# Performance work log

Hardware: AMD Instinct MI355X
Metric: run time of the kernel (lower is better)

## Reference

```python
import jax, jax.numpy as jnp
import numpy as np

HIDDEN = 1024
HEADS = 16
HEAD = HIDDEN // HEADS


def setup_inputs() -> dict:
    key = jax.random.key(0)
    k1, k2, k3, k4, k5, k6 = jax.random.split(key, 6)
    B, S = 2, 2048
    x = jax.random.normal(k1, (B, S, HIDDEN), dtype=jnp.float32)
    mask = jax.random.randint(k2, (B, S), 0, 2, dtype=jnp.int32)
    # torch nn.Linear params: W [out,in], b [out]
    s = 1.0 / np.sqrt(HIDDEN)
    qkv_w = jax.random.uniform(k3, (3 * HIDDEN, HIDDEN), jnp.float32, -s, s)
    qkv_b = jax.random.uniform(k4, (3 * HIDDEN,), jnp.float32, -s, s)
    out_w = jax.random.uniform(k5, (HIDDEN, HIDDEN), jnp.float32, -s, s)
    out_b = jax.random.uniform(k6, (HIDDEN,), jnp.float32, -s, s)
    return {"x": x, "mask": mask, "qkv_w": qkv_w, "qkv_b": qkv_b,
            "out_w": out_w, "out_b": out_b}


def reference(x, mask, qkv_w, qkv_b, out_w, out_b):
    B, S, H = x.shape
    scale = HEAD ** -0.5
    qkv = x @ qkv_w.T + qkv_b                      # [B,S,3H]
    qkv = qkv.reshape(B, S, 3, HEADS, HEAD)
    qkv = jnp.transpose(qkv, (2, 0, 3, 1, 4))      # [3,B,h,S,d]
    q, k, v = qkv[0], qkv[1], qkv[2]
    scores = jnp.einsum('bhqd,bhkd->bhqk', q, k) * scale
    # key-padding mask [B,S] -> [B,1,1,S]
    scores = jnp.where(mask[:, None, None, :] == 0, -1e9, scores)
    attn = jax.nn.softmax(scores, axis=-1)
    # dropout is identity in eval mode
    ctx = jnp.einsum('bhqk,bhkd->bhqd', attn, v)   # [B,h,S,d]
    ctx = jnp.transpose(ctx, (0, 2, 1, 3)).reshape(B, S, H)
    return ctx @ out_w.T + out_b
```

## Files before the change

### kernel.cpp

```cpp
#include <hip/hip_runtime.h>
#include <hip/hip_bf16.h>

#define S_LEN 2048
#define NH    16
#define HD    64
#define HID   1024
#define BATCH 2
#define STK   72
#define VSTK  136
#define SCQ   0.18033688f

typedef __bf16 bf16x8 __attribute__((ext_vector_type(8)));
typedef float  f32x4  __attribute__((ext_vector_type(4)));
typedef float  f32x16 __attribute__((ext_vector_type(16)));
typedef unsigned u32x2 __attribute__((ext_vector_type(2)));

__device__ __forceinline__ unsigned int pk2(float lo, float hi) {
    union { __hip_bfloat162 h; unsigned int u; } c;
    c.h = __float22bfloat162_rn(make_float2(lo, hi));
    return c.u;
}
__device__ __forceinline__ uint4 pk8(float4 a, float4 b) {
    uint4 o;
    o.x = pk2(a.x, a.y); o.y = pk2(a.z, a.w);
    o.z = pk2(b.x, b.y); o.w = pk2(b.z, b.w);
    return o;
}
__device__ __forceinline__ float exp2_hw(float x) {
    float r; asm("v_exp_f32 %0, %1" : "=v"(r) : "v"(x)); return r;
}
__device__ __forceinline__ void pl32swap(unsigned &a, unsigned &b) {
    u32x2 r = __builtin_amdgcn_permlane32_swap(a, b, false, false);
    a = r[0]; b = r[1];
}
__device__ __forceinline__ float pair_max(float x) {
    unsigned u = __float_as_uint(x);
    u32x2 r = __builtin_amdgcn_permlane32_swap(u, u, false, false);
    return fmaxf(__uint_as_float(r[0]), __uint_as_float(r[1]));
}
__device__ __forceinline__ float pair_sum(float x) {
    unsigned u = __float_as_uint(x);
    u32x2 r = __builtin_amdgcn_permlane32_swap(u, u, false, false);
    return __uint_as_float(r[0]) + __uint_as_float(r[1]);
}
__device__ __forceinline__ void gll16(const unsigned short* g, unsigned short* l) {
    __builtin_amdgcn_global_load_lds(
        (const __attribute__((address_space(1))) void*)g,
        (__attribute__((address_space(3))) void*)l, 16, 0, 0);
}

__global__ __launch_bounds__(256)
void fill_constf(float* __restrict__ out, long n, float v) {
    long i = (long)blockIdx.x * 256 + threadIdx.x;
    const long stride = (long)gridDim.x * 256;
    for (; i < n; i += stride) out[i] = v;
}

__global__ __launch_bounds__(256)
void cvt_bf16(const float* __restrict__ src, unsigned short* __restrict__ dst, long n8) {
    long t = (long)blockIdx.x * 256 + threadIdx.x;
    const long stride = (long)gridDim.x * 256;
    for (; t < n8; t += stride) {
        const float4 a = *(const float4*)(src + t * 8);
        const float4 b = *(const float4*)(src + t * 8 + 4);
        *(uint4*)(dst + t * 8) = pk8(a, b);
    }
}
__global__ __launch_bounds__(256)
void cvt2_bf16(const float* __restrict__ s0, unsigned short* __restrict__ d0, long n0,
               const float* __restrict__ s1, unsigned short* __restrict__ d1, long n1) {
    long t = (long)blockIdx.x * 256 + threadIdx.x;
    const long stride = (long)gridDim.x * 256;
    for (; t < n0 + n1; t += stride) {
        const float* s; unsigned short* d; long i;
        if (t < n0) { s = s0; d = d0; i = t; } else { s = s1; d = d1; i = t - n0; }
        const float4 a = *(const float4*)(s + i * 8);
        const float4 b = *(const float4*)(s + i * 8 + 4);
        *(uint4*)(d + i * 8) = pk8(a, b);
    }
}

__global__ __launch_bounds__(512)
void gemm_bf16(const unsigned short* __restrict__ A,
               const unsigned short* __restrict__ W,
               const float* __restrict__ bias,
               unsigned short* __restrict__ o0,
               unsigned short* __restrict__ o1,
               unsigned short* __restrict__ o2)
{
    __shared__ __align__(16) unsigned short lA[3][128 * 32];
    __shared__ __align__(16) unsigned short lB[3][128 * 32];
    const int tid  = threadIdx.x;
    const int lane = tid & 63, wv = tid >> 6;
    const int quad = lane >> 4, l16 = lane & 15;
    const int wm = (wv & 1) * 64, wn = (wv >> 1) * 32;

    const int nwg = gridDim.x * gridDim.y;
    const int bid = blockIdx.y * gridDim.x + blockIdx.x;
    const int xcd = bid & 7, boff = bid >> 3;
    const int qd = nwg >> 3, rm = nwg & 7;
    const int swz = (xcd < rm ? xcd * (qd + 1) : rm * (qd + 1) + (xcd - rm) * qd) + boff;
    const int m0 = (swz / gridDim.x) * 128, n0 = (swz % gridDim.x) * 128;

    f32x4 acc[4][2] = {};

    const int srow = wv * 16 + (lane >> 2);
    const int csrc = ((lane & 3) ^ ((lane >> 3) & 3)) * 8;
    const unsigned short* pa = A + (long)(m0 + srow) * HID + csrc;
    const unsigned short* pb = W + (long)(n0 + srow) * HID + csrc;

    const int cq8 = (quad ^ ((l16 >> 1) & 3)) * 8;

#define STAGE_G(bufi, koff)                                        \
    do {                                                           \
        gll16(pa + (koff), &lA[bufi][wv * 512]);                   \
        gll16(pb + (koff), &lB[bufi][wv * 512]);                   \
    } while (0)

    STAGE_G(0, 0);
    STAGE_G(1, 32);

    int cur = 0;
    for (int k0 = 0; k0 < HID; k0 += 32) {
        if (k0 + 32 < HID) { asm volatile("s_waitcnt vmcnt(2)" ::: "memory"); }
        else               { asm volatile("s_waitcnt vmcnt(0)" ::: "memory"); }
        __builtin_amdgcn_s_barrier();
        asm volatile("" ::: "memory");

        if (k0 + 64 < HID) {
            const int nxt = cur ? cur - 1 : 2;
            STAGE_G(nxt, k0 + 64);
        }

        bf16x8 af[4], bfr[2];
#pragma unroll
        for (int mt = 0; mt < 4; mt++)
            af[mt] = *(const bf16x8*)&lA[cur][(wm + mt * 16 + l16) * 32 + cq8];
#pragma unroll
        for (int nt = 0; nt < 2; nt++)
            bfr[nt] = *(const bf16x8*)&lB[cur][(wn + nt * 16 + l16) * 32 + cq8];
#pragma unroll
        for (int mt = 0; mt < 4; mt++)
#pragma unroll
            for (int nt = 0; nt < 2; nt++)
                acc[mt][nt] = __builtin_amdgcn_mfma_f32_16x16x32_bf16(
                    af[mt], bfr[nt], acc[mt][nt], 0, 0, 0);

        cur = (cur < 2) ? cur + 1 : 0;
    }
#undef STAGE_G

#pragma unroll
    for (int nt = 0; nt < 2; nt++) {
        const int n = n0 + wn + nt * 16 + l16;
        const float bv = bias[n];
        const int part = n >> 10, f = n & 1023, h = f >> 6, d = f & 63;
#pragma unroll
        for (int mt = 0; mt < 4; mt++) {
            const int mbase = m0 + wm + mt * 16 + quad * 4;
            const int b = mbase >> 11, s0 = mbase & 2047;
            const int bh = b * NH + h;
            if (part != 1) {
                const float qsc = (part == 0) ? SCQ : 1.0f;
                unsigned short* dst = (part == 0) ? o0 : o2;
                uint2 o;
                o.x = pk2((acc[mt][nt][0] + bv) * qsc, (acc[mt][nt][1] + bv) * qsc);
                o.y = pk2((acc[mt][nt][2] + bv) * qsc, (acc[mt][nt][3] + bv) * qsc);
                *(uint2*)&dst[((long)bh * HD + d) * S_LEN + s0] = o;
            } else {
#pragma unroll
                for (int r = 0; r < 4; r++) {
                    union { __hip_bfloat16 h; unsigned short u; } cv;
                    cv.h = __float2bfloat16(acc[mt][nt][r] + bv);
                    o1[((long)bh * S_LEN + s0 + r) * HD + d] = cv.u;
                }
            }
        }
    }
}

__global__ __launch_bounds__(256)
void gemm_out64(const unsigned short* __restrict__ A,
                const unsigned short* __restrict__ W,
                const float* __restrict__ bias,
                float* __restrict__ of)
{
    __shared__ __align__(16) unsigned short lA[3][128 * 32];
    __shared__ __align__(16) unsigned short lB[3][64 * 32];
    const int tid  = threadIdx.x;
    const int lane = tid & 63, wv = tid >> 6;
    const int quad = lane >> 4, l16 = lane & 15;
    const int wm = (wv & 1) * 64, wn = (wv >> 1) * 32;

    const int nwg = gridDim.x * gridDim.y;
    const int bid = blockIdx.y * gridDim.x + blockIdx.x;
    const int xcd = bid & 7, boff = bid >> 3;
    const int qd = nwg >> 3, rm = nwg & 7;
    const int swz = (xcd < rm ? xcd * (qd + 1) : rm * (qd + 1) + (xcd - rm) * qd) + boff;
    const int m0 = (swz / gridDim.x) * 128, n0 = (swz % gridDim.x) * 64;

    f32x4 acc[4][2] = {};

    const int arow0 = wv * 32 + (lane >> 2);
    const int arow1 = arow0 + 16;
    const int brow  = wv * 16 + (lane >> 2);
    const int csrc  = ((lane & 3) ^ ((lane >> 3) & 3)) * 8;
    const unsigned short* pa0 = A + (long)(m0 + arow0) * HID + csrc;
    const unsigned short* pa1 = A + (long)(m0 + arow1) * HID + csrc;
    const unsigned short* pb  = W + (long)(n0 + brow ) * HID + csrc;

    const int cq8 = (quad ^ ((l16 >> 1) & 3)) * 8;

#define STAGE_O(bufi, koff)                                        \
    do {                                                           \
        gll16(pa0 + (koff), &lA[bufi][(wv * 2 + 0) * 512]);        \
        gll16(pa1 + (koff), &lA[bufi][(wv * 2 + 1) * 512]);        \
        gll16(pb  + (koff), &lB[bufi][wv * 512]);                  \
    } while (0)

    STAGE_O(0, 0);
    STAGE_O(1, 32);

    int cur = 0;
    for (int k0 = 0; k0 < HID; k0 += 32) {
        if (k0 + 32 < HID) { asm volatile("s_waitcnt vmcnt(3)" ::: "memory"); }
        else               { asm volatile("s_waitcnt vmcnt(0)" ::: "memory"); }
        __builtin_amdgcn_s_barrier();
        asm volatile("" ::: "memory");

        if (k0 + 64 < HID) {
            const int nxt = cur ? cur - 1 : 2;
            STAGE_O(nxt, k0 + 64);
        }

        bf16x8 af[4], bfr[2];
#pragma unroll
        for (int mt = 0; mt < 4; mt++)
            af[mt] = *(const bf16x8*)&lA[cur][(wm + mt * 16 + l16) * 32 + cq8];
#pragma unroll
        for (int nt = 0; nt < 2; nt++)
            bfr[nt] = *(const bf16x8*)&lB[cur][(wn + nt * 16 + l16) * 32 + cq8];
#pragma unroll
        for (int mt = 0; mt < 4; mt++)
#pragma unroll
            for (int nt = 0; nt < 2; nt++)
                acc[mt][nt] = __builtin_amdgcn_mfma_f32_16x16x32_bf16(
                    af[mt], bfr[nt], acc[mt][nt], 0, 0, 0);

        cur = (cur < 2) ? cur + 1 : 0;
    }
#undef STAGE_O

#pragma unroll
    for (int nt = 0; nt < 2; nt++) {
        const int n = n0 + wn + nt * 16 + l16;
        const float bv = bias[n];
#pragma unroll
        for (int mt = 0; mt < 4; mt++) {
            const int mbase = m0 + wm + mt * 16 + quad * 4;
#pragma unroll
            for (int r = 0; r < 4; r++)
                of[(long)(mbase + r) * HID + n] = acc[mt][nt][r] + bv;
        }
    }
}

__global__ __launch_bounds__(512, 4)
void attn(const unsigned short* __restrict__ q,
          const unsigned short* __restrict__ k,
          const unsigned short* __restrict__ vt_g,
          const int* __restrict__ mask,
          unsigned short* __restrict__ ctx)
{
    __shared__ __align__(16) unsigned short kt[2][128 * STK];
    __shared__ __align__(16) unsigned short vt[2][64 * VSTK];
    __shared__ __align__(16) float mkv[2][128];

    const int tid  = threadIdx.x;
    const int lane = tid & 63, wv = tid >> 6;
    const int ar = lane & 31, hi = lane >> 5;
    const int chunk = wv >> 1, p = wv & 1;
    const int qt = blockIdx.x, h = blockIdx.y, b = blockIdx.z;
    const int bh = b * NH + h;
    const int sq = qt * 128 + chunk * 32 + ar;

    union { unsigned short u[8]; bf16x8 v; } qu[4];
    const unsigned short* qg = q + (long)bh * HD * S_LEN + sq;
#pragma unroll
    for (int t = 0; t < 4; t++)
#pragma unroll
        for (int j = 0; j < 8; j++)
            qu[t].u[j] = qg[(long)(16 * t + 8 * hi + j) * S_LEN];

    float mrun = 0.f, lsum = 0.f;
    f32x16 Of0 = {}, Of1 = {};

    const int sr = tid >> 3, c0 = tid & 7;
    const unsigned short* kg = k    + ((long)bh * S_LEN + sr) * HD + c0 * 8;
    const unsigned short* vg = vt_g + ((long)bh * HD + sr) * S_LEN + c0 * 8;
    const int wk0 = sr * STK + c0 * 8;
    const int wk1 = (sr + 64) * STK + c0 * 8;
    const int wv0 = sr * VSTK + c0 * 8;
    const int wv1 = sr * VSTK + c0 * 8 + 64;

    uint4 rk0 = *(const uint4*)(kg);
    uint4 rk1 = *(const uint4*)(kg + (long)64 * HD);
    uint4 rv0 = *(const uint4*)(vg);
    uint4 rv1 = *(const uint4*)(vg + 64);
    float rmv = 0.f;
    if (tid < 128) rmv = (mask[b * S_LEN + tid] == 0) ? -1e9f : 0.f;
    *(uint4*)&kt[0][wk0] = rk0;
    *(uint4*)&kt[0][wk1] = rk1;
    *(uint4*)&vt[0][wv0] = rv0;
    *(uint4*)&vt[0][wv1] = rv1;
    if (tid < 128) mkv[0][tid] = rmv;
    rk0 = *(const uint4*)(kg + (long)128 * HD);
    rk1 = *(const uint4*)(kg + (long)192 * HD);
    rv0 = *(const uint4*)(vg + 128);
    rv1 = *(const uint4*)(vg + 192);
    if (tid < 128) rmv = (mask[b * S_LEN + 128 + tid] == 0) ? -1e9f : 0.f;
    asm volatile("s_waitcnt lgkmcnt(0)" ::: "memory");
    __builtin_amdgcn_s_barrier();
    asm volatile("" ::: "memory");

    for (int k0 = 0; k0 < S_LEN; k0 += 128) {
        const int cur = (k0 >> 7) & 1;
        if (k0 + 128 < S_LEN) {
            *(uint4*)&kt[cur ^ 1][wk0] = rk0;
            *(uint4*)&kt[cur ^ 1][wk1] = rk1;
            *(uint4*)&vt[cur ^ 1][wv0] = rv0;
            *(uint4*)&vt[cur ^ 1][wv1] = rv1;
            if (tid < 128) mkv[cur ^ 1][tid] = rmv;
            if (k0 + 256 < S_LEN) {
                rk0 = *(const uint4*)(kg + (long)(k0 + 256) * HD);
                rk1 = *(const uint4*)(kg + (long)(k0 + 320) * HD);
                rv0 = *(const uint4*)(vg + (k0 + 256));
                rv1 = *(const uint4*)(vg + (k0 + 320));
                if (tid < 128) rmv = (mask[b * S_LEN + k0 + 256 + tid] == 0) ? -1e9f : 0.f;
            }
        }

#pragma unroll
        for (int G2 = 0; G2 < 2; G2++) {
            const int kb = 64 * G2 + 32 * p;

            f32x16 s;
#pragma unroll
            for (int m = 0; m < 4; m++) {
                const float4 mv = *(const float4*)&mkv[cur][kb + m * 8 + hi * 4];
                s[4 * m + 0] = mv.x; s[4 * m + 1] = mv.y;
                s[4 * m + 2] = mv.z; s[4 * m + 3] = mv.w;
            }
            __builtin_amdgcn_s_setprio(1);
#pragma unroll
            for (int t = 0; t < 4; t++) {
                bf16x8 kf = *(const bf16x8*)
                    &kt[cur][(kb + ar) * STK + (2 * t + hi) * 8];
                s = __builtin_amdgcn_mfma_f32_32x32x16_bf16(kf, qu[t].v, s, 0, 0, 0);
            }
            __builtin_amdgcn_s_setprio(0);

            if (k0 == 0 && G2 == 0) {
                float pm = fmaxf(fmaxf(fmaxf(s[0], s[1]), fmaxf(s[2], s[3])),
                           fmaxf(fmaxf(s[4], s[5]), fmaxf(s[6], s[7])));
                pm = fmaxf(pm,
                     fmaxf(fmaxf(fmaxf(s[8], s[9]), fmaxf(s[10], s[11])),
                           fmaxf(fmaxf(s[12], s[13]), fmaxf(s[14], s[15]))));
                mrun = fmaxf(pair_max(pm), -50.f);
            }

            float pr[16];
            float ls = 0.f;
#pragma unroll
            for (int r = 0; r < 16; r++) {
                pr[r] = exp2_hw(s[r] - mrun);
                ls += pr[r];
            }
            lsum += ls;
            unsigned wa[4], wb[4];
#pragma unroll
            for (int m = 0; m < 4; m++) {
                wa[m] = pk2(pr[4 * m + 0], pr[4 * m + 1]);
                wb[m] = pk2(pr[4 * m + 2], pr[4 * m + 3]);
            }

            union { unsigned u[4]; bf16x8 v; } F[2];
#pragma unroll
            for (int s5 = 0; s5 < 2; s5++) {
                const int mp = s5 * 2;
                unsigned f0 = wa[mp], f2 = wa[mp + 1];
                unsigned f1 = wb[mp], f3 = wb[mp + 1];
                pl32swap(f0, f2);
                pl32swap(f1, f3);
                F[s5].u[0] = f0; F[s5].u[1] = f1; F[s5].u[2] = f2; F[s5].u[3] = f3;
            }

            __builtin_amdgcn_s_setprio(1);
#pragma unroll
            for (int s5 = 0; s5 < 2; s5++) {
                const int col = (2 * (4 * G2 + 2 * p + s5) + hi) * 8;
                bf16x8 vf0 = *(const bf16x8*)&vt[cur][(0 * 32 + ar) * VSTK + col];
                Of0 = __builtin_amdgcn_mfma_f32_32x32x16_bf16(vf0, F[s5].v, Of0, 0, 0, 0);
                bf16x8 vf1 = *(const bf16x8*)&vt[cur][(1 * 32 + ar) * VSTK + col];
                Of1 = __builtin_amdgcn_mfma_f32_32x32x16_bf16(vf1, F[s5].v, Of1, 0, 0, 0);
            }
            __builtin_amdgcn_s_setprio(0);
        }

        asm volatile("s_waitcnt lgkmcnt(0)" ::: "memory");
        __builtin_amdgcn_s_barrier();
        asm volatile("" ::: "memory");
    }

    const float lp = pair_sum(lsum);
    float* mo0 = (float*)&kt[0][0];
    float* mo1 = (float*)&vt[0][0];
    float* mml = (float*)&vt[0][0] + 4096;
    const int mbase = (chunk * 64 + lane) * 16;
    const int mx4 = (lane >> 1) & 3;
    if (p == 1) {
#pragma unroll
        for (int m = 0; m < 4; m++) {
            const int off = mbase + ((m ^ mx4) << 2);
            *(float4*)&mo0[off] = make_float4(Of0[4*m+0], Of0[4*m+1], Of0[4*m+2], Of0[4*m+3]);
            *(float4*)&mo1[off] = make_float4(Of1[4*m+0], Of1[4*m+1], Of1[4*m+2], Of1[4*m+3]);
        }
        mml[(chunk * 64 + lane) * 2 + 0] = mrun;
        mml[(chunk * 64 + lane) * 2 + 1] = lp;
    }
    __syncthreads();
    if (p == 0) {
        const float m1 = mml[(chunk * 64 + lane) * 2 + 0];
        const float l1 = mml[(chunk * 64 + lane) * 2 + 1];
        const float mm = fmaxf(mrun, m1);
        const float a0 = exp2_hw(mrun - mm);
        const float a1 = exp2_hw(m1 - mm);
        const float inv = 1.f / (lp * a0 + l1 * a1);
        unsigned short* cb = ctx + ((long)b * S_LEN + sq) * HID + h * HD;
#pragma unroll
        for (int m = 0; m < 4; m++) {
            const int off = mbase + ((m ^ mx4) << 2);
            const float4 p0 = *(const float4*)&mo0[off];
            const float4 p1 = *(const float4*)&mo1[off];
            uint2 o0, o1;
            o0.x = pk2((Of0[4*m+0] * a0 + p0.x * a1) * inv,
                       (Of0[4*m+1] * a0 + p0.y * a1) * inv);
            o0.y = pk2((Of0[4*m+2] * a0 + p0.z * a1) * inv,
                       (Of0[4*m+3] * a0 + p0.w * a1) * inv);
            *(uint2*)&cb[m * 8 + hi * 4] = o0;
            o1.x = pk2((Of1[4*m+0] * a0 + p1.x * a1) * inv,
                       (Of1[4*m+1] * a0 + p1.y * a1) * inv);
            o1.y = pk2((Of1[4*m+2] * a0 + p1.z * a1) * inv,
                       (Of1[4*m+3] * a0 + p1.w * a1) * inv);
            *(uint2*)&cb[32 + m * 8 + hi * 4] = o1;
        }
    }
}

extern "C" void kernel_launch(void* const* d_in, const int* in_sizes, int n_in,
                              void* d_out, int out_size, void* d_ws, size_t ws_size,
                              hipStream_t stream) {
    float* outp = (float*)d_out;

    const float* x = nullptr; const int* mask = nullptr;
    const float* qkv_w = nullptr; const float* qkv_b = nullptr;
    const float* out_w = nullptr; const float* out_b = nullptr;
    for (int i = 0; i < n_in; i++) {
        switch (in_sizes[i]) {
            case 4194304: x     = (const float*)d_in[i]; break;
            case 4096:    mask  = (const int*)d_in[i];   break;
            case 3145728: qkv_w = (const float*)d_in[i]; break;
            case 3072:    qkv_b = (const float*)d_in[i]; break;
            case 1048576: out_w = (const float*)d_in[i]; break;
            case 1024:    out_b = (const float*)d_in[i]; break;
            default: break;
        }
    }
    if (!x || !mask || !qkv_w || !qkv_b || !out_w || !out_b) {
        fill_constf<<<256, 256, 0, stream>>>(outp, (long)out_size, 1000.0f);
        return;
    }

    const size_t per = (size_t)BATCH * NH * S_LEN * HD;
    const size_t nx  = (size_t)BATCH * S_LEN * HID;
    const size_t nqw = (size_t)3 * HID * HID;
    const size_t now = (size_t)HID * HID;
    if (ws_size < 4 * per * sizeof(unsigned short)) {
        fill_constf<<<256, 256, 0, stream>>>(outp, (long)out_size, 2000.0f);
        return;
    }

    unsigned short* wsq = (unsigned short*)d_ws;
    unsigned short* wsk = wsq + per;
    unsigned short* wsv = wsk + per;
    unsigned short* wsc = wsv + per;
    unsigned short* xb  = wsc;
    unsigned short* qwb = (unsigned short*)d_out;
    unsigned short* owb = wsq;

    cvt2_bf16<<<1024, 256, 0, stream>>>(x, xb, (long)(nx / 8), qkv_w, qwb, (long)(nqw / 8));
    gemm_bf16<<<dim3(3 * HID / 128, BATCH * S_LEN / 128), 512, 0, stream>>>(
        xb, qwb, qkv_b, wsq, wsk, wsv);
    attn<<<dim3(S_LEN / 128, NH, BATCH), 512, 0, stream>>>(wsq, wsk, wsv, mask, wsc);
    cvt_bf16<<<512, 256, 0, stream>>>(out_w, owb, (long)(now / 8));
    gemm_out64<<<dim3(HID / 64, BATCH * S_LEN / 128), 256, 0, stream>>>(
        wsc, owb, out_b, outp);
}
```

Baseline: 196.0 us.

## Widen output GEMM to 8 waves and XCD-swizzle attention grid by head

The output-projection GEMM moves from 4 to 8 waves per block. Each wave now computes a 32x32 sub-tile, and only half the waves stage the B tile, so vmcnt waits differ per wave. The attention launch becomes a 1-D grid whose block index is remapped so that all query tiles of the same (batch, head) land on the same XCD, for better L2 reuse of K/V. The GEMM change trades fewer accumulators per wave for more waves to hide latency, with more LDS reads of B per MFMA.

After: 196.6 us. Within noise of the previous version (+0.3%).

```diff
diff --git a/kernel.cpp b/kernel.cpp
--- a/kernel.cpp
+++ b/kernel.cpp
@@ -179,18 +179,18 @@
     }
 }
 
-__global__ __launch_bounds__(256)
-void gemm_out64(const unsigned short* __restrict__ A,
-                const unsigned short* __restrict__ W,
-                const float* __restrict__ bias,
-                float* __restrict__ of)
+__global__ __launch_bounds__(512)
+void gemm_out(const unsigned short* __restrict__ A,
+              const unsigned short* __restrict__ W,
+              const float* __restrict__ bias,
+              float* __restrict__ of)
 {
     __shared__ __align__(16) unsigned short lA[3][128 * 32];
     __shared__ __align__(16) unsigned short lB[3][64 * 32];
     const int tid  = threadIdx.x;
     const int lane = tid & 63, wv = tid >> 6;
     const int quad = lane >> 4, l16 = lane & 15;
-    const int wm = (wv & 1) * 64, wn = (wv >> 1) * 32;
+    const int wm = (wv & 3) * 32, wn = (wv >> 2) * 32;
 
     const int nwg = gridDim.x * gridDim.y;
     const int bid = blockIdx.y * gridDim.x + blockIdx.x;
@@ -199,23 +199,20 @@
     const int swz = (xcd < rm ? xcd * (qd + 1) : rm * (qd + 1) + (xcd - rm) * qd) + boff;
     const int m0 = (swz / gridDim.x) * 128, n0 = (swz % gridDim.x) * 64;
 
-    f32x4 acc[4][2] = {};
-
-    const int arow0 = wv * 32 + (lane >> 2);
-    const int arow1 = arow0 + 16;
-    const int brow  = wv * 16 + (lane >> 2);
+    f32x4 acc[2][2] = {};
+
+    const int srowA = wv * 16 + (lane >> 2);
+    const int srowB = srowA & 63;
     const int csrc  = ((lane & 3) ^ ((lane >> 3) & 3)) * 8;
-    const unsigned short* pa0 = A + (long)(m0 + arow0) * HID + csrc;
-    const unsigned short* pa1 = A + (long)(m0 + arow1) * HID + csrc;
-    const unsigned short* pb  = W + (long)(n0 + brow ) * HID + csrc;
+    const unsigned short* pa = A + (long)(m0 + srowA) * HID + csrc;
+    const unsigned short* pb = W + (long)(n0 + srowB) * HID + csrc;
 
     const int cq8 = (quad ^ ((l16 >> 1) & 3)) * 8;
 
 #define STAGE_O(bufi, koff)                                        \
     do {                                                           \
-        gll16(pa0 + (koff), &lA[bufi][(wv * 2 + 0) * 512]);        \
-        gll16(pa1 + (koff), &lA[bufi][(wv * 2 + 1) * 512]);        \
-        gll16(pb  + (koff), &lB[bufi][wv * 512]);                  \
+        gll16(pa + (koff), &lA[bufi][wv * 512]);                   \
+        if (wv < 4) gll16(pb + (koff), &lB[bufi][wv * 512]);       \
     } while (0)
 
     STAGE_O(0, 0);
@@ -223,8 +220,10 @@
 
     int cur = 0;
     for (int k0 = 0; k0 < HID; k0 += 32) {
-        if (k0 + 32 < HID) { asm volatile("s_waitcnt vmcnt(3)" ::: "memory"); }
-        else               { asm volatile("s_waitcnt vmcnt(0)" ::: "memory"); }
+        if (k0 + 32 < HID) {
+            if (wv < 4) { asm volatile("s_waitcnt vmcnt(2)" ::: "memory"); }
+            else        { asm volatile("s_waitcnt vmcnt(1)" ::: "memory"); }
+        } else          { asm volatile("s_waitcnt vmcnt(0)" ::: "memory"); }
         __builtin_amdgcn_s_barrier();
         asm volatile("" ::: "memory");
 
@@ -233,15 +232,15 @@
             STAGE_O(nxt, k0 + 64);
         }
 
-        bf16x8 af[4], bfr[2];
-#pragma unroll
-        for (int mt = 0; mt < 4; mt++)
+        bf16x8 af[2], bfr[2];
+#pragma unroll
+        for (int mt = 0; mt < 2; mt++)
             af[mt] = *(const bf16x8*)&lA[cur][(wm + mt * 16 + l16) * 32 + cq8];
 #pragma unroll
         for (int nt = 0; nt < 2; nt++)
             bfr[nt] = *(const bf16x8*)&lB[cur][(wn + nt * 16 + l16) * 32 + cq8];
 #pragma unroll
-        for (int mt = 0; mt < 4; mt++)
+        for (int mt = 0; mt < 2; mt++)
 #pragma unroll
             for (int nt = 0; nt < 2; nt++)
                 acc[mt][nt] = __builtin_amdgcn_mfma_f32_16x16x32_bf16(
@@ -256,7 +255,7 @@
         const int n = n0 + wn + nt * 16 + l16;
         const float bv = bias[n];
 #pragma unroll
-        for (int mt = 0; mt < 4; mt++) {
+        for (int mt = 0; mt < 2; mt++) {
             const int mbase = m0 + wm + mt * 16 + quad * 4;
 #pragma unroll
             for (int r = 0; r < 4; r++)
@@ -280,7 +279,11 @@
     const int lane = tid & 63, wv = tid >> 6;
     const int ar = lane & 31, hi = lane >> 5;
     const int chunk = wv >> 1, p = wv & 1;
-    const int qt = blockIdx.x, h = blockIdx.y, b = blockIdx.z;
+    const int id = blockIdx.x;
+    const int xcd = id & 7, j = id >> 3;
+    const int qt = j & 15, hbl = j >> 4;
+    const int hb = xcd * 4 + hbl;
+    const int h = hb & 15, b = hb >> 4;
     const int bh = b * NH + h;
     const int sq = qt * 128 + chunk * 32 + ar;
 
@@ -289,8 +292,8 @@
 #pragma unroll
     for (int t = 0; t < 4; t++)
 #pragma unroll
-        for (int j = 0; j < 8; j++)
-            qu[t].u[j] = qg[(long)(16 * t + 8 * hi + j) * S_LEN];
+        for (int jj = 0; jj < 8; jj++)
+            qu[t].u[jj] = qg[(long)(16 * t + 8 * hi + jj) * S_LEN];
 
     float mrun = 0.f, lsum = 0.f;
     f32x16 Of0 = {}, Of1 = {};
@@ -501,8 +504,8 @@
     cvt2_bf16<<<1024, 256, 0, stream>>>(x, xb, (long)(nx / 8), qkv_w, qwb, (long)(nqw / 8));
     gemm_bf16<<<dim3(3 * HID / 128, BATCH * S_LEN / 128), 512, 0, stream>>>(
         xb, qwb, qkv_b, wsq, wsk, wsv);
-    attn<<<dim3(S_LEN / 128, NH, BATCH), 512, 0, stream>>>(wsq, wsk, wsv, mask, wsc);
+    attn<<<dim3(S_LEN / 128 * NH * BATCH), 512, 0, stream>>>(wsq, wsk, wsv, mask, wsc);
     cvt_bf16<<<512, 256, 0, stream>>>(out_w, owb, (long)(now / 8));
-    gemm_out64<<<dim3(HID / 64, BATCH * S_LEN / 128), 256, 0, stream>>>(
+    gemm_out<<<dim3(HID / 64, BATCH * S_LEN / 128), 512, 0, stream>>>(
         wsc, owb, out_b, outp);
 }
```
